# Kernel tuning notes

Measured on AMD Instinct MI355X. Metric: run time of the kernel, lower is better.

## Reference

```python
import jax, jax.numpy as jnp
import numpy as np

S, B, D, H = 2048, 2, 1024, 16
DK = D // H  # 64

def setup_inputs() -> dict:
    key0 = jax.random.key(0)
    ks = jax.random.split(key0, 11)
    scale = 0.02
    inp = {
        'query': jax.random.normal(ks[0], (S, B, D), jnp.float32),
        'key':   jax.random.normal(ks[1], (S, B, D), jnp.float32),
        'value': jax.random.normal(ks[2], (S, B, D), jnp.float32),
        # nn.Linear weights stored torch-style [out_features, in_features]
        'Wq': jax.random.normal(ks[3], (H * DK, D), jnp.float32) * scale,
        'bq': jnp.zeros((H * DK,), jnp.float32),
        'Wk': jax.random.normal(ks[4], (H * DK, D), jnp.float32) * scale,
        'bk': jnp.zeros((H * DK,), jnp.float32),
        'Wv': jax.random.normal(ks[5], (H * DK, D), jnp.float32) * scale,
        'bv': jnp.zeros((H * DK,), jnp.float32),
        'Wo': jax.random.normal(ks[6], (D, D), jnp.float32) * scale,
        'bo': jnp.zeros((D,), jnp.float32),
    }
    return inp

def _proj(x, W, b):
    # x: [S,B,D] -> [S,B,H,DK]
    y = jnp.einsum('sbd,ed->sbe', x, W) + b
    return y.reshape(x.shape[0], x.shape[1], H, DK)

def reference(query, key, value, Wq, bq, Wk, bk, Wv, bv, Wo, bo):
    q = _proj(query, Wq, bq)   # [S,B,H,DK]
    k = _proj(key,   Wk, bk)
    v = _proj(value, Wv, bv)
    # NOTE: original forward never applies self.scale -> unscaled QK^T (faithful)
    scores = jnp.einsum('ibhd,jbhd->ijbh', q, k)      # [Sq,Sk,B,H]
    attn = jax.nn.softmax(scores, axis=1)             # softmax over key axis j
    x = jnp.einsum('ijbh,jbhd->ibhd', attn, v)        # [S,B,H,DK]
    x = x.reshape(q.shape[0], q.shape[1], H * DK)     # [S,B,D]
    out = jnp.einsum('sbd,ed->sbe', x, Wo) + bo       # [S,B,D]
    return out
```

## Files before the change

### kernel.cpp

```cpp
#include <hip/hip_runtime.h>
#include <stdint.h>

#define S_LEN  2048
#define BATCH  2
#define DMODEL 1024
#define NHEAD  16
#define DKH    64

typedef __attribute__((ext_vector_type(8))) __bf16 bf16x8;
typedef __attribute__((ext_vector_type(4))) float  f32x4;
typedef unsigned short u16;
typedef unsigned int   u32;

__device__ __forceinline__ u16 f2bf(float f) {
  union { float f; u32 u; } v; v.f = f;
  u32 r = v.u + 0x7fffu + ((v.u >> 16) & 1u);
  return (u16)(r >> 16);
}

__global__ void cvt3_kernel(const float4* __restrict__ a, const float4* __restrict__ b,
                            const float4* __restrict__ c,
                            ushort4* __restrict__ oa, ushort4* __restrict__ ob,
                            ushort4* __restrict__ oc, int n4) {
  int i = blockIdx.x * blockDim.x + threadIdx.x;
  if (i >= n4) return;
  const float4* src = (blockIdx.y == 0) ? a : (blockIdx.y == 1) ? b : c;
  ushort4*      dst = (blockIdx.y == 0) ? oa : (blockIdx.y == 1) ? ob : oc;
  float4 v = src[i];
  ushort4 o;
  o.x = f2bf(v.x); o.y = f2bf(v.y); o.z = f2bf(v.z); o.w = f2bf(v.w);
  dst[i] = o;
}

__global__ void cvt4_kernel(const float4* __restrict__ a, const float4* __restrict__ b,
                            const float4* __restrict__ c, const float4* __restrict__ d,
                            ushort4* __restrict__ oa, ushort4* __restrict__ ob,
                            ushort4* __restrict__ oc, ushort4* __restrict__ od, int n4) {
  int i = blockIdx.x * blockDim.x + threadIdx.x;
  if (i >= n4) return;
  const float4* src = (blockIdx.y == 0) ? a : (blockIdx.y == 1) ? b : (blockIdx.y == 2) ? c : d;
  ushort4*      dst = (blockIdx.y == 0) ? oa : (blockIdx.y == 1) ? ob : (blockIdx.y == 2) ? oc : od;
  float4 v = src[i];
  ushort4 o;
  o.x = f2bf(v.x); o.y = f2bf(v.y); o.z = f2bf(v.z); o.w = f2bf(v.w);
  dst[i] = o;
}

__global__ __launch_bounds__(256, 2)
void gemm_qkv(const u16* __restrict__ Abase, const u16* __restrict__ Wbase,
              const float* __restrict__ b0, const float* __restrict__ b1,
              const float* __restrict__ b2, u16* __restrict__ Obase) {
  __shared__ __align__(16) u16 As[128 * 32];
  __shared__ __align__(16) u16 Bs[128 * 32];

  const int z = blockIdx.z;
  const u16* A = Abase + (size_t)z * (S_LEN * BATCH * DMODEL);
  const u16* W = Wbase + (size_t)z * (DMODEL * DMODEL);
  const float* bias = (z == 0) ? b0 : (z == 1) ? b1 : b2;
  u16* O = Obase + (size_t)z * (S_LEN * BATCH * DMODEL);

  const int tid  = threadIdx.x;
  const int wave = tid >> 6, lane = tid & 63;
  const int quad = lane >> 4, lcol = lane & 15;
  const int m0 = blockIdx.y * 128, n0 = blockIdx.x * 128;
  const int wm = (wave >> 1) * 64, wn = (wave & 1) * 64;

  f32x4 acc[4][4] = {};

  for (int k0 = 0; k0 < DMODEL; k0 += 32) {
#pragma unroll
    for (int r = 0; r < 2; ++r) {
      int idx = r * 256 + tid;
      int row = idx >> 2, col = (idx & 3) * 8;
      const u16* gA = A + (size_t)(m0 + row) * DMODEL + k0 + col;
      const u16* gW = W + (size_t)(n0 + row) * DMODEL + k0 + col;
      u16* lA = As + (size_t)(r * 256 + (tid & 192)) * 8;
      u16* lB = Bs + (size_t)(r * 256 + (tid & 192)) * 8;
      __builtin_amdgcn_global_load_lds((const __attribute__((address_space(1))) void*)gA,
                                       (__attribute__((address_space(3))) void*)lA, 16, 0, 0);
      __builtin_amdgcn_global_load_lds((const __attribute__((address_space(1))) void*)gW,
                                       (__attribute__((address_space(3))) void*)lB, 16, 0, 0);
    }
    __syncthreads();

    const u16* aBase = As + (wm + lcol) * 32 + quad * 8;
    const u16* bBase = Bs + (wn + lcol) * 32 + quad * 8;
    bf16x8 af[4], bfr[4];
#pragma unroll
    for (int i = 0; i < 4; ++i) af[i]  = *(const bf16x8*)(aBase + i * 16 * 32);
#pragma unroll
    for (int j = 0; j < 4; ++j) bfr[j] = *(const bf16x8*)(bBase + j * 16 * 32);
#pragma unroll
    for (int i = 0; i < 4; ++i)
#pragma unroll
      for (int j = 0; j < 4; ++j)
        acc[i][j] = __builtin_amdgcn_mfma_f32_16x16x32_bf16(af[i], bfr[j], acc[i][j], 0, 0, 0);
    __syncthreads();
  }

#pragma unroll
  for (int i = 0; i < 4; ++i) {
#pragma unroll
    for (int j = 0; j < 4; ++j) {
      int n = n0 + wn + j * 16 + lcol;
      int h = n >> 6, dk = n & 63;
      float bv = bias[n];
#pragma unroll
      for (int r = 0; r < 4; ++r) {
        int m = m0 + wm + i * 16 + quad * 4 + r;
        int s = m >> 1, b = m & 1;
        O[((size_t)(b * NHEAD + h) * S_LEN + s) * DKH + dk] = f2bf(acc[i][j][r] + bv);
      }
    }
  }
}

__global__ __launch_bounds__(256, 2)
void gemm_o(const u16* __restrict__ A, const u16* __restrict__ W,
            const float* __restrict__ bias, float* __restrict__ O) {
  __shared__ __align__(16) u16 As[128 * 32];
  __shared__ __align__(16) u16 Bs[64 * 32];

  const int tid  = threadIdx.x;
  const int wave = tid >> 6, lane = tid & 63;
  const int quad = lane >> 4, lcol = lane & 15;
  const int m0 = blockIdx.y * 128, n0 = blockIdx.x * 64;
  const int wm = (wave >> 1) * 64, wn = (wave & 1) * 32;

  f32x4 acc[4][2] = {};

  for (int k0 = 0; k0 < DMODEL; k0 += 32) {
#pragma unroll
    for (int r = 0; r < 2; ++r) {
      int idx = r * 256 + tid;
      int row = idx >> 2, col = (idx & 3) * 8;
      const u16* gA = A + (size_t)(m0 + row) * DMODEL + k0 + col;
      u16* lA = As + (size_t)(r * 256 + (tid & 192)) * 8;
      __builtin_amdgcn_global_load_lds((const __attribute__((address_space(1))) void*)gA,
                                       (__attribute__((address_space(3))) void*)lA, 16, 0, 0);
    }
    {
      int row = tid >> 2, col = (tid & 3) * 8;
      const u16* gW = W + (size_t)(n0 + row) * DMODEL + k0 + col;
      u16* lB = Bs + (size_t)(tid & 192) * 8;
      __builtin_amdgcn_global_load_lds((const __attribute__((address_space(1))) void*)gW,
                                       (__attribute__((address_space(3))) void*)lB, 16, 0, 0);
    }
    __syncthreads();

    const u16* aBase = As + (wm + lcol) * 32 + quad * 8;
    const u16* bBase = Bs + (wn + lcol) * 32 + quad * 8;
    bf16x8 af[4], bfr[2];
#pragma unroll
    for (int i = 0; i < 4; ++i) af[i]  = *(const bf16x8*)(aBase + i * 16 * 32);
#pragma unroll
    for (int j = 0; j < 2; ++j) bfr[j] = *(const bf16x8*)(bBase + j * 16 * 32);
#pragma unroll
    for (int i = 0; i < 4; ++i)
#pragma unroll
      for (int j = 0; j < 2; ++j)
        acc[i][j] = __builtin_amdgcn_mfma_f32_16x16x32_bf16(af[i], bfr[j], acc[i][j], 0, 0, 0);
    __syncthreads();
  }

#pragma unroll
  for (int i = 0; i < 4; ++i) {
#pragma unroll
    for (int j = 0; j < 2; ++j) {
      int n = n0 + wn + j * 16 + lcol;
      float bv = bias[n];
#pragma unroll
      for (int r = 0; r < 4; ++r) {
        int m = m0 + wm + i * 16 + quad * 4 + r;
        O[(size_t)m * DMODEL + n] = acc[i][j][r] + bv;
      }
    }
  }
}

__global__ __launch_bounds__(256, 3)
void attn_kernel(const u16* __restrict__ Q, const u16* __restrict__ K,
                 const u16* __restrict__ V, u16* __restrict__ O) {
  __shared__ __align__(16) u16 Ks[64 * 72];
  __shared__ __align__(16) u16 Vts[64 * 72];
  __shared__ __align__(16) u16 Ps[4][32 * 72];
  __shared__ float l_s[128];

  const int tid  = threadIdx.x;
  const int wave = tid >> 6, lane = tid & 63;
  const int quad = lane >> 4, lcol = lane & 15;
  const int bh = blockIdx.y;
  const int q0 = blockIdx.x * 128;

  const size_t headOff = (size_t)bh * S_LEN * DKH;
  const u16* Qg = Q + headOff;
  const u16* Kg = K + headOff;
  const u16* Vg = V + headOff;

  bf16x8 qf[2][2];
#pragma unroll
  for (int s = 0; s < 2; ++s)
#pragma unroll
    for (int ks = 0; ks < 2; ++ks)
      qf[s][ks] = *(const bf16x8*)(Qg + (size_t)(q0 + wave * 32 + s * 16 + lcol) * DKH +
                                   ks * 32 + quad * 8);

  f32x4 o_acc[2][4] = {};
  float lsum[2] = {0.f, 0.f};

  const int vkp = tid & 31;
  const int vo  = tid >> 5;

  for (int kt = 0; kt < S_LEN; kt += 64) {
    __syncthreads();
#pragma unroll
    for (int r = 0; r < 2; ++r) {
      int idx = r * 256 + tid;
      int row = idx >> 3, c0 = (idx & 7) * 8;
      *(uint4*)(Ks + row * 72 + c0) = *(const uint4*)(Kg + (size_t)(kt + row) * DKH + c0);
    }
    {
      const u16* vp = Vg + (size_t)(kt + 2 * vkp) * DKH + 8 * vo;
      uint4 va = *(const uint4*)vp;
      uint4 vb = *(const uint4*)(vp + DKH);
      const u16* pa = (const u16*)&va;
      const u16* pb = (const u16*)&vb;
#pragma unroll
      for (int jj = 0; jj < 8; ++jj) {
        u32 w = (u32)pa[jj] | ((u32)pb[jj] << 16);
        *(u32*)(Vts + (size_t)(8 * vo + jj) * 72 + 2 * vkp) = w;
      }
    }
    __syncthreads();

    f32x4 sc[2][4] = {};
#pragma unroll
    for (int ks = 0; ks < 2; ++ks) {
      bf16x8 ak[4];
#pragma unroll
      for (int j = 0; j < 4; ++j)
        ak[j] = *(const bf16x8*)(Ks + (j * 16 + lcol) * 72 + ks * 32 + quad * 8);
#pragma unroll
      for (int s = 0; s < 2; ++s)
#pragma unroll
        for (int j = 0; j < 4; ++j)
          sc[s][j] = __builtin_amdgcn_mfma_f32_16x16x32_bf16(ak[j], qf[s][ks], sc[s][j], 0, 0, 0);
    }

#pragma unroll
    for (int s = 0; s < 2; ++s) {
      u16* prow = Ps[wave] + (s * 16 + lcol) * 72;
#pragma unroll
      for (int j = 0; j < 4; ++j) {
        float p0 = __expf(sc[s][j][0]);
        float p1 = __expf(sc[s][j][1]);
        float p2 = __expf(sc[s][j][2]);
        float p3 = __expf(sc[s][j][3]);
        lsum[s] += (p0 + p1) + (p2 + p3);
        u32 w0 = (u32)f2bf(p0) | ((u32)f2bf(p1) << 16);
        u32 w1 = (u32)f2bf(p2) | ((u32)f2bf(p3) << 16);
        uint2 pk; pk.x = w0; pk.y = w1;
        *(uint2*)(prow + j * 16 + quad * 4) = pk;
      }
    }

#pragma unroll
    for (int ks = 0; ks < 2; ++ks) {
      bf16x8 bv[4];
#pragma unroll
      for (int jd = 0; jd < 4; ++jd)
        bv[jd] = *(const bf16x8*)(Vts + (jd * 16 + lcol) * 72 + ks * 32 + quad * 8);
#pragma unroll
      for (int s = 0; s < 2; ++s) {
        bf16x8 ap = *(const bf16x8*)(Ps[wave] + (s * 16 + lcol) * 72 + ks * 32 + quad * 8);
#pragma unroll
        for (int jd = 0; jd < 4; ++jd)
          o_acc[s][jd] = __builtin_amdgcn_mfma_f32_16x16x32_bf16(ap, bv[jd], o_acc[s][jd], 0, 0, 0);
      }
    }
  }

#pragma unroll
  for (int s = 0; s < 2; ++s) {
    lsum[s] += __shfl_xor(lsum[s], 16);
    lsum[s] += __shfl_xor(lsum[s], 32);
  }
  if (lane < 16) {
    l_s[wave * 32 + lane]      = lsum[0];
    l_s[wave * 32 + 16 + lane] = lsum[1];
  }
  __syncthreads();

  const int b = bh >> 4, h = bh & 15;
#pragma unroll
  for (int s = 0; s < 2; ++s) {
#pragma unroll
    for (int r = 0; r < 4; ++r) {
      float inv = 1.f / l_s[wave * 32 + s * 16 + quad * 4 + r];
      int sq = q0 + wave * 32 + s * 16 + quad * 4 + r;
#pragma unroll
      for (int jd = 0; jd < 4; ++jd) {
        int dk = jd * 16 + lcol;
        O[((size_t)(sq * BATCH + b)) * DMODEL + h * DKH + dk] = f2bf(o_acc[s][jd][r] * inv);
      }
    }
  }
}

extern "C" void kernel_launch(void* const* d_in, const int* in_sizes, int n_in,
                              void* d_out, int out_size, void* d_ws, size_t ws_size,
                              hipStream_t stream) {
  const float* q  = (const float*)d_in[0];
  const float* k  = (const float*)d_in[1];
  const float* v  = (const float*)d_in[2];
  const float* Wq = (const float*)d_in[3];
  const float* bq = (const float*)d_in[4];
  const float* Wk = (const float*)d_in[5];
  const float* bk = (const float*)d_in[6];
  const float* Wv = (const float*)d_in[7];
  const float* bv = (const float*)d_in[8];
  const float* Wo = (const float*)d_in[9];
  const float* bo = (const float*)d_in[10];

  const int NX = S_LEN * BATCH * DMODEL;
  const int NW = DMODEL * DMODEL;

  u16* ws  = (u16*)d_ws;
  u16* Xq  = ws;
  u16* Wqb = Xq  + 3 * (size_t)NX;
  u16* Qb  = Wqb + 4 * (size_t)NW;
  u16* Xo  = Qb  + 3 * (size_t)NX;

  u16* Xk  = Xq + NX, *Xv = Xq + 2 * (size_t)NX;
  u16* Wkb = Wqb + NW, *Wvb = Wqb + 2 * (size_t)NW, *Wob = Wqb + 3 * (size_t)NW;
  u16* Kb  = Qb + NX, *Vb = Qb + 2 * (size_t)NX;

  dim3 g3(NX / 4 / 256, 3);
  cvt3_kernel<<<g3, 256, 0, stream>>>((const float4*)q, (const float4*)k, (const float4*)v,
                                      (ushort4*)Xq, (ushort4*)Xk, (ushort4*)Xv, NX / 4);
  dim3 g4(NW / 4 / 256, 4);
  cvt4_kernel<<<g4, 256, 0, stream>>>((const float4*)Wq, (const float4*)Wk, (const float4*)Wv,
                                      (const float4*)Wo,
                                      (ushort4*)Wqb, (ushort4*)Wkb, (ushort4*)Wvb, (ushort4*)Wob,
                                      NW / 4);

  dim3 gqkv(DMODEL / 128, (S_LEN * BATCH) / 128, 3);
  gemm_qkv<<<gqkv, 256, 0, stream>>>(Xq, Wqb, bq, bk, bv, Qb);

  dim3 ga(S_LEN / 128, BATCH * NHEAD);
  attn_kernel<<<ga, 256, 0, stream>>>(Qb, Kb, Vb, Xo);

  dim3 go(DMODEL / 64, (S_LEN * BATCH) / 128);
  gemm_o<<<go, 256, 0, stream>>>(Xo, Wob, bo, (float*)d_out);
}
```

Before: 248.8 us.

## Widen attention key tile to 128, prefetch next K/V into registers, merge conversion kernels

```diff
diff --git a/kernel.cpp b/kernel.cpp
--- a/kernel.cpp
+++ b/kernel.cpp
@@ -18,32 +18,20 @@
   return (u16)(r >> 16);
 }
 
-__global__ void cvt3_kernel(const float4* __restrict__ a, const float4* __restrict__ b,
-                            const float4* __restrict__ c,
-                            ushort4* __restrict__ oa, ushort4* __restrict__ ob,
-                            ushort4* __restrict__ oc, int n4) {
+struct CvtPtrs {
+  const float4* src[7];
+  ushort4*      dst[7];
+  int           n4[7];
+};
+
+__global__ void cvt_all(CvtPtrs p) {
+  int t = blockIdx.y;
   int i = blockIdx.x * blockDim.x + threadIdx.x;
-  if (i >= n4) return;
-  const float4* src = (blockIdx.y == 0) ? a : (blockIdx.y == 1) ? b : c;
-  ushort4*      dst = (blockIdx.y == 0) ? oa : (blockIdx.y == 1) ? ob : oc;
-  float4 v = src[i];
+  if (i >= p.n4[t]) return;
+  float4 v = p.src[t][i];
   ushort4 o;
   o.x = f2bf(v.x); o.y = f2bf(v.y); o.z = f2bf(v.z); o.w = f2bf(v.w);
-  dst[i] = o;
-}
-
-__global__ void cvt4_kernel(const float4* __restrict__ a, const float4* __restrict__ b,
-                            const float4* __restrict__ c, const float4* __restrict__ d,
-                            ushort4* __restrict__ oa, ushort4* __restrict__ ob,
-                            ushort4* __restrict__ oc, ushort4* __restrict__ od, int n4) {
-  int i = blockIdx.x * blockDim.x + threadIdx.x;
-  if (i >= n4) return;
-  const float4* src = (blockIdx.y == 0) ? a : (blockIdx.y == 1) ? b : (blockIdx.y == 2) ? c : d;
-  ushort4*      dst = (blockIdx.y == 0) ? oa : (blockIdx.y == 1) ? ob : (blockIdx.y == 2) ? oc : od;
-  float4 v = src[i];
-  ushort4 o;
-  o.x = f2bf(v.x); o.y = f2bf(v.y); o.z = f2bf(v.z); o.w = f2bf(v.w);
-  dst[i] = o;
+  p.dst[t][i] = o;
 }
 
 __global__ __launch_bounds__(256, 2)
@@ -178,12 +166,12 @@
   }
 }
 
-__global__ __launch_bounds__(256, 3)
+__global__ __launch_bounds__(256, 2)
 void attn_kernel(const u16* __restrict__ Q, const u16* __restrict__ K,
                  const u16* __restrict__ V, u16* __restrict__ O) {
-  __shared__ __align__(16) u16 Ks[64 * 72];
-  __shared__ __align__(16) u16 Vts[64 * 72];
-  __shared__ __align__(16) u16 Ps[4][32 * 72];
+  __shared__ __align__(16) u16 Ks[128 * 72];
+  __shared__ __align__(16) u16 Vts[64 * 136];
+  __shared__ __align__(16) u16 Ps[4][32 * 136];
   __shared__ float l_s[128];
 
   const int tid  = threadIdx.x;
@@ -208,71 +196,98 @@
   f32x4 o_acc[2][4] = {};
   float lsum[2] = {0.f, 0.f};
 
-  const int vkp = tid & 31;
-  const int vo  = tid >> 5;
-
-  for (int kt = 0; kt < S_LEN; kt += 64) {
-    __syncthreads();
-#pragma unroll
-    for (int r = 0; r < 2; ++r) {
+  const int vkp = lane;
+  const int vo  = wave;
+
+  uint4 kr[4], vr[4];
+#pragma unroll
+  for (int r = 0; r < 4; ++r) {
+    int idx = r * 256 + tid;
+    kr[r] = *(const uint4*)(Kg + (size_t)(idx >> 3) * DKH + (idx & 7) * 8);
+  }
+  {
+    const u16* vp = Vg + (size_t)(2 * vkp) * DKH + 8 * vo;
+    vr[0] = *(const uint4*)vp;
+    vr[1] = *(const uint4*)(vp + DKH);
+    vr[2] = *(const uint4*)(vp + 32);
+    vr[3] = *(const uint4*)(vp + 32 + DKH);
+  }
+
+  for (int kt = 0; kt < S_LEN; kt += 128) {
+    __syncthreads();
+#pragma unroll
+    for (int r = 0; r < 4; ++r) {
       int idx = r * 256 + tid;
-      int row = idx >> 3, c0 = (idx & 7) * 8;
-      *(uint4*)(Ks + row * 72 + c0) = *(const uint4*)(Kg + (size_t)(kt + row) * DKH + c0);
+      *(uint4*)(Ks + (idx >> 3) * 72 + (idx & 7) * 8) = kr[r];
     }
     {
-      const u16* vp = Vg + (size_t)(kt + 2 * vkp) * DKH + 8 * vo;
-      uint4 va = *(const uint4*)vp;
-      uint4 vb = *(const uint4*)(vp + DKH);
-      const u16* pa = (const u16*)&va;
-      const u16* pb = (const u16*)&vb;
+      const u16* pa0 = (const u16*)&vr[0];
+      const u16* pb0 = (const u16*)&vr[1];
+      const u16* pa1 = (const u16*)&vr[2];
+      const u16* pb1 = (const u16*)&vr[3];
 #pragma unroll
       for (int jj = 0; jj < 8; ++jj) {
-        u32 w = (u32)pa[jj] | ((u32)pb[jj] << 16);
-        *(u32*)(Vts + (size_t)(8 * vo + jj) * 72 + 2 * vkp) = w;
-      }
-    }
-    __syncthreads();
-
-    f32x4 sc[2][4] = {};
+        u32 w0 = (u32)pa0[jj] | ((u32)pb0[jj] << 16);
+        *(u32*)(Vts + (size_t)(8 * vo + jj) * 136 + 2 * vkp) = w0;
+        u32 w1 = (u32)pa1[jj] | ((u32)pb1[jj] << 16);
+        *(u32*)(Vts + (size_t)(8 * vo + 32 + jj) * 136 + 2 * vkp) = w1;
+      }
+    }
+    __syncthreads();
+
+    if (kt + 128 < S_LEN) {
+      const u16* Kn = Kg + (size_t)(kt + 128) * DKH;
+#pragma unroll
+      for (int r = 0; r < 4; ++r) {
+        int idx = r * 256 + tid;
+        kr[r] = *(const uint4*)(Kn + (size_t)(idx >> 3) * DKH + (idx & 7) * 8);
+      }
+      const u16* vp = Vg + (size_t)(kt + 128 + 2 * vkp) * DKH + 8 * vo;
+      vr[0] = *(const uint4*)vp;
+      vr[1] = *(const uint4*)(vp + DKH);
+      vr[2] = *(const uint4*)(vp + 32);
+      vr[3] = *(const uint4*)(vp + 32 + DKH);
+    }
+
+    f32x4 sc[2][8] = {};
 #pragma unroll
     for (int ks = 0; ks < 2; ++ks) {
-      bf16x8 ak[4];
-#pragma unroll
-      for (int j = 0; j < 4; ++j)
-        ak[j] = *(const bf16x8*)(Ks + (j * 16 + lcol) * 72 + ks * 32 + quad * 8);
-#pragma unroll
-      for (int s = 0; s < 2; ++s)
-#pragma unroll
-        for (int j = 0; j < 4; ++j)
-          sc[s][j] = __builtin_amdgcn_mfma_f32_16x16x32_bf16(ak[j], qf[s][ks], sc[s][j], 0, 0, 0);
+#pragma unroll
+      for (int j = 0; j < 8; ++j) {
+        bf16x8 ak = *(const bf16x8*)(Ks + (j * 16 + lcol) * 72 + ks * 32 + quad * 8);
+        sc[0][j] = __builtin_amdgcn_mfma_f32_16x16x32_bf16(ak, qf[0][ks], sc[0][j], 0, 0, 0);
+        sc[1][j] = __builtin_amdgcn_mfma_f32_16x16x32_bf16(ak, qf[1][ks], sc[1][j], 0, 0, 0);
+      }
     }
 
 #pragma unroll
     for (int s = 0; s < 2; ++s) {
-      u16* prow = Ps[wave] + (s * 16 + lcol) * 72;
-#pragma unroll
-      for (int j = 0; j < 4; ++j) {
+      u16* prow = Ps[wave] + (s * 16 + lcol) * 136;
+#pragma unroll
+      for (int j = 0; j < 8; ++j) {
         float p0 = __expf(sc[s][j][0]);
         float p1 = __expf(sc[s][j][1]);
         float p2 = __expf(sc[s][j][2]);
         float p3 = __expf(sc[s][j][3]);
         lsum[s] += (p0 + p1) + (p2 + p3);
-        u32 w0 = (u32)f2bf(p0) | ((u32)f2bf(p1) << 16);
-        u32 w1 = (u32)f2bf(p2) | ((u32)f2bf(p3) << 16);
-        uint2 pk; pk.x = w0; pk.y = w1;
+        uint2 pk;
+        pk.x = (u32)f2bf(p0) | ((u32)f2bf(p1) << 16);
+        pk.y = (u32)f2bf(p2) | ((u32)f2bf(p3) << 16);
         *(uint2*)(prow + j * 16 + quad * 4) = pk;
       }
     }
 
-#pragma unroll
-    for (int ks = 0; ks < 2; ++ks) {
+    __syncthreads();
+
+#pragma unroll
+    for (int kc = 0; kc < 4; ++kc) {
       bf16x8 bv[4];
 #pragma unroll
       for (int jd = 0; jd < 4; ++jd)
-        bv[jd] = *(const bf16x8*)(Vts + (jd * 16 + lcol) * 72 + ks * 32 + quad * 8);
+        bv[jd] = *(const bf16x8*)(Vts + (jd * 16 + lcol) * 136 + kc * 32 + quad * 8);
 #pragma unroll
       for (int s = 0; s < 2; ++s) {
-        bf16x8 ap = *(const bf16x8*)(Ps[wave] + (s * 16 + lcol) * 72 + ks * 32 + quad * 8);
+        bf16x8 ap = *(const bf16x8*)(Ps[wave] + (s * 16 + lcol) * 136 + kc * 32 + quad * 8);
 #pragma unroll
         for (int jd = 0; jd < 4; ++jd)
           o_acc[s][jd] = __builtin_amdgcn_mfma_f32_16x16x32_bf16(ap, bv[jd], o_acc[s][jd], 0, 0, 0);
@@ -335,14 +350,17 @@
   u16* Wkb = Wqb + NW, *Wvb = Wqb + 2 * (size_t)NW, *Wob = Wqb + 3 * (size_t)NW;
   u16* Kb  = Qb + NX, *Vb = Qb + 2 * (size_t)NX;
 
-  dim3 g3(NX / 4 / 256, 3);
-  cvt3_kernel<<<g3, 256, 0, stream>>>((const float4*)q, (const float4*)k, (const float4*)v,
-                                      (ushort4*)Xq, (ushort4*)Xk, (ushort4*)Xv, NX / 4);
-  dim3 g4(NW / 4 / 256, 4);
-  cvt4_kernel<<<g4, 256, 0, stream>>>((const float4*)Wq, (const float4*)Wk, (const float4*)Wv,
-                                      (const float4*)Wo,
-                                      (ushort4*)Wqb, (ushort4*)Wkb, (ushort4*)Wvb, (ushort4*)Wob,
-                                      NW / 4);
+  CvtPtrs cp;
+  cp.src[0] = (const float4*)q;  cp.dst[0] = (ushort4*)Xq;  cp.n4[0] = NX / 4;
+  cp.src[1] = (const float4*)k;  cp.dst[1] = (ushort4*)Xk;  cp.n4[1] = NX / 4;
+  cp.src[2] = (const float4*)v;  cp.dst[2] = (ushort4*)Xv;  cp.n4[2] = NX / 4;
+  cp.src[3] = (const float4*)Wq; cp.dst[3] = (ushort4*)Wqb; cp.n4[3] = NW / 4;
+  cp.src[4] = (const float4*)Wk; cp.dst[4] = (ushort4*)Wkb; cp.n4[4] = NW / 4;
+  cp.src[5] = (const float4*)Wv; cp.dst[5] = (ushort4*)Wvb; cp.n4[5] = NW / 4;
+  cp.src[6] = (const float4*)Wo; cp.dst[6] = (ushort4*)Wob; cp.n4[6] = NW / 4;
+
+  dim3 gc(NX / 4 / 256, 7);
+  cvt_all<<<gc, 256, 0, stream>>>(cp);
 
   dim3 gqkv(DMODEL / 128, (S_LEN * BATCH) / 128, 3);
   gemm_qkv<<<gqkv, 256, 0, stream>>>(Xq, Wqb, bq, bk, bv, Qb);
```

After: 253.7 us. No clear change (+1.9%).
